# Optimization experiments

Hardware: AMD Instinct MI355X
Metric: run time of the kernel (lower is better)

The kernel has to match this reference:

```python
import jax, jax.numpy as jnp
import numpy as np

T, B, L, D, A = 64, 64, 100, 128, 18
H = 4 * D  # lstm_size = 4 * input_size


def lstm_cell(x, h, c, Wih, Whh, bih, bhh):
    # PyTorch LSTM gate order: i, f, g, o
    g = x @ Wih.T + bih + h @ Whh.T + bhh
    i, f, gg, o = jnp.split(g, 4, axis=-1)
    c = jax.nn.sigmoid(f) * c + jax.nn.sigmoid(i) * jnp.tanh(gg)
    h = jax.nn.sigmoid(o) * jnp.tanh(c)
    return h, c


def setup_inputs() -> dict:
    key = jax.random.key(0)
    ks = jax.random.split(key, 26)

    def gl(k, shape, fan_in):
        s = float(1.0 / np.sqrt(fan_in))
        return jax.random.uniform(k, shape, jnp.float32, -s, s)

    return dict(
        state=jax.random.normal(ks[0], (T, B, D), jnp.float32),
        demonstration=jax.random.normal(ks[1], (T, B, L, D), jnp.float32),
        demonstration_length=jax.random.randint(ks[2], (T, B), 1, L + 1),
        prev_action=jax.random.randint(ks[3], (T, B), 0, A),
        prev_reward=jax.random.normal(ks[4], (T, B), jnp.float32),
        h0=jnp.zeros((B, H), jnp.float32),
        c0=jnp.zeros((B, H), jnp.float32),
        enc_Wih=gl(ks[5], (4 * H, D), H), enc_Whh=gl(ks[6], (4 * H, H), H),
        enc_bih=gl(ks[7], (4 * H,), H), enc_bhh=gl(ks[8], (4 * H,), H),
        attn_W=gl(ks[9], (H, H), H), attn_b=gl(ks[10], (H,), H),
        comb_W=gl(ks[11], (H, D + H), D + H), comb_b=gl(ks[12], (H,), D + H),
        lstm_Wih=gl(ks[13], (4 * H, H), H), lstm_Whh=gl(ks[14], (4 * H, H), H),
        lstm_bih=gl(ks[15], (4 * H,), H), lstm_bhh=gl(ks[16], (4 * H,), H),
        mid_W=gl(ks[17], (H, H), H), mid_b=gl(ks[18], (H,), H),
        out_W=gl(ks[19], (A, H), H), out_b=gl(ks[20], (A,), H),
    )


def reference(state, demonstration, demonstration_length, prev_action, prev_reward,
              h0, c0, enc_Wih, enc_Whh, enc_bih, enc_bhh, attn_W, attn_b,
              comb_W, comb_b, lstm_Wih, lstm_Whh, lstm_bih, lstm_bhh,
              mid_W, mid_b, out_W, out_b):
    Lm = demonstration.shape[2]
    demo0 = demonstration[0]  # [B, L, D] (source uses demonstration[0] only)

    # --- demonstration encoder LSTM over L, zero initial state ---
    def enc_step(carry, x):
        h, c = carry
        h, c = lstm_cell(x, h, c, enc_Wih, enc_Whh, enc_bih, enc_bhh)
        return (h, c), h

    z = jnp.zeros((demo0.shape[0], H), demo0.dtype)
    _, enc = jax.lax.scan(enc_step, (z, z), jnp.swapaxes(demo0, 0, 1))
    enc = jnp.swapaxes(enc, 0, 1)  # [B, L, H]

    # invariant across t in the source loop; hoisted (same math)
    attn_proj = enc @ attn_W.T + attn_b  # [B, L, H]
    lengths = demonstration_length[0]  # [B]
    mask = jnp.arange(Lm)[None, :] < lengths[:, None]  # [B, L]
    scale = jnp.float32(1.0 / np.sqrt(Lm))

    # --- per-timestep fused attention + LSTM cell + heads ---
    def step(carry, obs_t):
        h, c = carry
        w = jnp.einsum('blh,bh->bl', attn_proj, h) * scale
        w = jnp.where(mask, w, -jnp.inf)
        w = jax.nn.softmax(w, axis=-1)
        applied = jnp.einsum('bl,blh->bh', w, enc)
        x = jax.nn.relu(jnp.concatenate([applied, obs_t], axis=-1) @ comb_W.T + comb_b)
        h, c = lstm_cell(x, h, c, lstm_Wih, lstm_Whh, lstm_bih, lstm_bhh)
        m = h @ mid_W.T + mid_b
        q_t = m @ out_W.T + out_b
        return (h, c), q_t

    (h, c), q = jax.lax.scan(step, (h0, c0), state)  # q: [T, B, A]
    return q, h, c
```

## Files before the change

### kernel.cpp

```cpp
#include <hip/hip_runtime.h>
#include <math.h>

#define Bsz 64
#define Tn 64
#define Ln 100
#define Dn 128
#define An 18
#define Hn 512
#define NGRP 16

__device__ __forceinline__ float sigf(float x){ return 1.0f/(1.0f+expf(-x)); }

__device__ __forceinline__ void scst(float* p, float v){
  __hip_atomic_store(p, v, __ATOMIC_RELAXED, __HIP_MEMORY_SCOPE_AGENT);
}
__device__ __forceinline__ void scsti(int* p, int v){
  __hip_atomic_store(p, v, __ATOMIC_RELAXED, __HIP_MEMORY_SCOPE_AGENT);
}
__device__ __forceinline__ int lcldi(const int* p){
  return __hip_atomic_load((int*)p, __ATOMIC_RELAXED, __HIP_MEMORY_SCOPE_AGENT);
}

__device__ __forceinline__ void gbar_arrive(int* grp_arr, int* grp_gen, int* root, int nb, int ph){
  const int gs = nb >> 4;
  const int g  = (int)blockIdx.x & 15;
  int a = __hip_atomic_fetch_add(grp_arr + g*64, 1, __ATOMIC_RELAXED, __HIP_MEMORY_SCOPE_AGENT) + 1;
  if (a == ph*gs){
    int r = __hip_atomic_fetch_add(root, 1, __ATOMIC_RELAXED, __HIP_MEMORY_SCOPE_AGENT) + 1;
    if (r == ph*NGRP){
      #pragma unroll
      for (int i = 0; i < NGRP; i++) scsti(grp_gen + i*64, ph);
    }
  }
}
__device__ __forceinline__ void gbar_wait(int* grp_gen, int ph){
  const int g = (int)blockIdx.x & 15;
  while (lcldi(grp_gen + g*64) < ph) __builtin_amdgcn_s_sleep(1);
}
__device__ __forceinline__ void gbarH(int* gA, int* gG, int* gR, int nb, int ph){
  __syncthreads();
  if (threadIdx.x == 0){
    asm volatile("s_waitcnt vmcnt(0) lgkmcnt(0)" ::: "memory");
    gbar_arrive(gA, gG, gR, nb, ph);
    gbar_wait(gG, ph);
  }
  __syncthreads();
}

__global__ __launch_bounds__(256) void demo_transpose_kernel(
    const float* __restrict__ demo, float* __restrict__ demoT)
{
  int idx = blockIdx.x*256 + threadIdx.x;
  if (idx < Ln*Bsz*Dn) {
    int d = idx & 127;
    int b = (idx >> 7) & 63;
    int l = idx >> 13;
    demoT[idx] = demo[((size_t)(b*Ln + l))*Dn + d];
  }
}

__global__ __launch_bounds__(256) void gemm_nt_kernel(
    const float* __restrict__ A, int lda,
    const float* __restrict__ B, int ldb,
    const float* __restrict__ bias,
    float* __restrict__ C, int ldc, int K)
{
  __shared__ float As[64][17];
  __shared__ float Bs[64][17];
  const int m0 = blockIdx.x * 64;
  const int n0 = blockIdx.y * 64;
  const int tx = threadIdx.x & 15;
  const int ty = threadIdx.x >> 4;
  float acc[4][4] = {};
  for (int k0 = 0; k0 < K; k0 += 16) {
    #pragma unroll
    for (int i = 0; i < 4; i++) {
      int e = threadIdx.x + i*256;
      int r = e >> 4, c = e & 15;
      As[r][c] = A[(size_t)(m0 + r)*lda + k0 + c];
      Bs[r][c] = B[(size_t)(n0 + r)*ldb + k0 + c];
    }
    __syncthreads();
    #pragma unroll
    for (int kk = 0; kk < 16; kk++) {
      float a0 = As[ty*4+0][kk], a1 = As[ty*4+1][kk], a2 = As[ty*4+2][kk], a3 = As[ty*4+3][kk];
      float b0 = Bs[tx*4+0][kk], b1 = Bs[tx*4+1][kk], b2 = Bs[tx*4+2][kk], b3 = Bs[tx*4+3][kk];
      acc[0][0] += a0*b0; acc[0][1] += a0*b1; acc[0][2] += a0*b2; acc[0][3] += a0*b3;
      acc[1][0] += a1*b0; acc[1][1] += a1*b1; acc[1][2] += a1*b2; acc[1][3] += a1*b3;
      acc[2][0] += a2*b0; acc[2][1] += a2*b1; acc[2][2] += a2*b2; acc[2][3] += a2*b3;
      acc[3][0] += a3*b0; acc[3][1] += a3*b1; acc[3][2] += a3*b2; acc[3][3] += a3*b3;
    }
    __syncthreads();
  }
  #pragma unroll
  for (int i = 0; i < 4; i++) {
    #pragma unroll
    for (int j = 0; j < 4; j++) {
      int nn = n0 + tx*4 + j;
      float v = acc[i][j] + (bias ? bias[nn] : 0.0f);
      C[(size_t)(m0 + ty*4 + i)*ldc + nn] = v;
    }
  }
}

__global__ __launch_bounds__(512) void head_fold_kernel(
    const float* __restrict__ mid_W, const float* __restrict__ mid_b,
    const float* __restrict__ out_W, const float* __restrict__ out_b,
    float* __restrict__ M2, float* __restrict__ bias2)
{
  const int a = blockIdx.x;
  const int k = threadIdx.x;
  const float* ow = out_W + (size_t)a*Hn;
  float s = 0.f;
  #pragma unroll 4
  for (int n = 0; n < Hn; n++) s += ow[n]*mid_W[(size_t)n*Hn + k];
  M2[(size_t)a*Hn + k] = s;
  if (k == 0){
    float b2 = out_b[a];
    for (int n = 0; n < Hn; n++) b2 += ow[n]*mid_b[n];
    bias2[a] = b2;
  }
}

__global__ __launch_bounds__(256) void qhead_kernel(
    const float* __restrict__ hhist, const float* __restrict__ M2,
    const float* __restrict__ bias2, float* __restrict__ q)
{
  const int t = blockIdx.x;
  for (int p = threadIdx.x; p < Bsz*An; p += 256){
    int b = p / An, a = p % An;
    const float4* hv = (const float4*)(hhist + ((size_t)t*Bsz + b)*Hn);
    const float4* mv = (const float4*)(M2 + (size_t)a*Hn);
    float s = bias2[a];
    #pragma unroll 8
    for (int k = 0; k < Hn/4; k++){
      float4 H = hv[k], M = mv[k];
      s += H.x*M.x + H.y*M.y + H.z*M.z + H.w*M.w;
    }
    q[((size_t)(t*Bsz + b))*An + a] = s;
  }
}

__global__ __launch_bounds__(512, 1) void enc_scan_kernel(
    const float* __restrict__ demoT,
    const float* __restrict__ Wih, const float* __restrict__ Whh,
    const float* __restrict__ bih, const float* __restrict__ bhh,
    const float* __restrict__ attn_W, const float* __restrict__ attn_b,
    const float* __restrict__ comb_W,
    float* __restrict__ hencR,
    float* __restrict__ attnp,
    float* __restrict__ CE,
    int* __restrict__ gA, int* __restrict__ gG, int* __restrict__ gR)
{
  const int bid  = blockIdx.x;
  const int tid  = threadIdx.x;
  const int lane = tid & 63;
  const int ks   = tid >> 6;
  const int n0   = bid*2;

  __shared__ float lds_whh[8][Hn];
  __shared__ float lds_wih[8][Dn];
  __shared__ float lds_atw[2][Hn];
  __shared__ float lds_cbw[2][Hn];
  __shared__ float red[8][12][Bsz];

  #pragma unroll
  for (int c = 0; c < 2; c++)
    #pragma unroll
    for (int g = 0; g < 4; g++){
      int r = c*4 + g;
      lds_whh[r][tid] = Whh[(size_t)(g*Hn + n0 + c)*Hn + tid];
      if (tid < Dn) lds_wih[r][tid] = Wih[(size_t)(g*Hn + n0 + c)*Dn + tid];
    }
  #pragma unroll
  for (int c = 0; c < 2; c++){
    lds_atw[c][tid] = attn_W[(size_t)(n0 + c)*Hn + tid];
    lds_cbw[c][tid] = comb_W[(size_t)(n0 + c)*(Hn + Dn) + tid];
  }
  float bsum[2][4];
  #pragma unroll
  for (int c = 0; c < 2; c++)
    #pragma unroll
    for (int g = 0; g < 4; g++){
      int r = g*Hn + n0 + c;
      bsum[c][g] = bih[r] + bhh[r];
    }
  const float ab[2] = { attn_b[n0], attn_b[n0+1] };
  float cr[2] = {0.f, 0.f};
  __syncthreads();

  for (int l = 0; l <= Ln; l++){
    float a[2][4] = {{0,0,0,0},{0,0,0,0}};
    float aa[2] = {0,0}, ac[2] = {0,0};
    if (l >= 1){
      const float4* hv = (const float4*)(hencR + ((size_t)(l-1)*Bsz + lane)*Hn) + ks*16;
      #pragma unroll 4
      for (int q = 0; q < 16; q++){
        float4 H = hv[q];
        #pragma unroll
        for (int c = 0; c < 2; c++){
          #pragma unroll
          for (int g = 0; g < 4; g++){
            float4 W = *(const float4*)&lds_whh[c*4+g][ks*64 + 4*q];
            a[c][g] += H.x*W.x + H.y*W.y + H.z*W.z + H.w*W.w;
          }
          float4 Aw = *(const float4*)&lds_atw[c][ks*64 + 4*q];
          aa[c] += H.x*Aw.x + H.y*Aw.y + H.z*Aw.z + H.w*Aw.w;
          float4 Cw = *(const float4*)&lds_cbw[c][ks*64 + 4*q];
          ac[c] += H.x*Cw.x + H.y*Cw.y + H.z*Cw.z + H.w*Cw.w;
        }
      }
    }
    if (l < Ln){
      const float4* dv = (const float4*)(demoT + ((size_t)l*Bsz + lane)*Dn) + ks*4;
      #pragma unroll
      for (int q = 0; q < 4; q++){
        float4 V = dv[q];
        #pragma unroll
        for (int c = 0; c < 2; c++)
          #pragma unroll
          for (int g = 0; g < 4; g++){
            float4 W = *(const float4*)&lds_wih[c*4+g][ks*16 + 4*q];
            a[c][g] += V.x*W.x + V.y*W.y + V.z*W.z + V.w*W.w;
          }
      }
    }
    #pragma unroll
    for (int c = 0; c < 2; c++){
      #pragma unroll
      for (int g = 0; g < 4; g++) red[ks][c*4+g][lane] = a[c][g];
      red[ks][8+c][lane]  = aa[c];
      red[ks][10+c][lane] = ac[c];
    }
    __syncthreads();
    if (tid < Bsz){
      int b = tid;
      if (l < Ln){
        #pragma unroll
        for (int c = 0; c < 2; c++){
          float g0 = bsum[c][0], g1 = bsum[c][1], g2 = bsum[c][2], g3 = bsum[c][3];
          #pragma unroll
          for (int k = 0; k < 8; k++){
            g0 += red[k][c*4+0][b]; g1 += red[k][c*4+1][b];
            g2 += red[k][c*4+2][b]; g3 += red[k][c*4+3][b];
          }
          float ii = sigf(g0), ff = sigf(g1), gg = tanhf(g2), oo = sigf(g3);
          float cn = ff*cr[c] + ii*gg;
          float hn = oo*tanhf(cn);
          cr[c] = cn;
          scst(hencR + ((size_t)l*Bsz + b)*Hn + n0 + c, hn);
        }
      }
      if (l >= 1){
        #pragma unroll
        for (int c = 0; c < 2; c++){
          float av = ab[c], cv = 0.f;
          #pragma unroll
          for (int k = 0; k < 8; k++){ av += red[k][8+c][b]; cv += red[k][10+c][b]; }
          scst(attnp + ((size_t)(b*Ln + (l-1)))*Hn + n0 + c, av);
          scst(CE    + ((size_t)(b*Ln + (l-1)))*Hn + n0 + c, cv);
        }
      }
    }
    if (l < Ln) gbarH(gA, gG, gR, (int)gridDim.x, l+1);
  }
}

__global__ __launch_bounds__(512, 1) void dec_scan_kernel(
    const float* __restrict__ h0, const float* __restrict__ c0,
    const float* __restrict__ attnp,
    const float* __restrict__ CE,
    const float* __restrict__ preobs,
    const int*   __restrict__ dlen,
    const float* __restrict__ lstm_Wih, const float* __restrict__ lstm_Whh,
    const float* __restrict__ lstm_bih, const float* __restrict__ lstm_bhh,
    const float* __restrict__ comb_b,
    float* __restrict__ xrow,
    float* __restrict__ hhist,
    float* __restrict__ outp,
    int* __restrict__ gA, int* __restrict__ gG, int* __restrict__ gR)
{
  const int bid  = blockIdx.x;
  const int tid  = threadIdx.x;
  const int lane = tid & 63;
  const int ks   = tid >> 6;
  const int n0   = bid*2;

  __shared__ float lds_wi[8][Hn];
  __shared__ float lds_wh[8][Hn];
  __shared__ float hs[Hn];
  __shared__ float wls[128];
  __shared__ float mx_s, sum_s;
  __shared__ float red[8][8][Bsz];

  #pragma unroll
  for (int c = 0; c < 2; c++)
    #pragma unroll
    for (int g = 0; g < 4; g++){
      int r = c*4 + g;
      lds_wi[r][tid] = lstm_Wih[(size_t)(g*Hn + n0 + c)*Hn + tid];
      lds_wh[r][tid] = lstm_Whh[(size_t)(g*Hn + n0 + c)*Hn + tid];
    }
  float bs[2][4];
  #pragma unroll
  for (int c = 0; c < 2; c++)
    #pragma unroll
    for (int g = 0; g < 4; g++){
      int r = g*Hn + n0 + c;
      bs[c][g] = lstm_bih[r] + lstm_bhh[r];
    }
  float cr[2] = {0.f, 0.f};
  int len = 0, lenr = 0;
  if (bid < Bsz){ len = dlen[bid]; lenr = (len + 7) & ~7; }
  int ph = 0;
  __syncthreads();

  for (int t = 0; t < Tn; t++){
    const float* hprev_all = (t == 0) ? h0 : (hhist + (size_t)(t-1)*Bsz*Hn);

    if (bid < Bsz){
      const int b = bid;
      hs[tid] = hprev_all[(size_t)b*Hn + tid];
      if (tid >= 100 && tid < 128) wls[tid] = -1e30f;
      __syncthreads();
      if (tid < 400){
        int l = tid >> 2, kh = tid & 3;
        const float4* ap = (const float4*)(attnp + ((size_t)(b*Ln + l))*Hn) + kh*32;
        const float4* hv = (const float4*)hs + kh*32;
        float s = 0.f;
        #pragma unroll 8
        for (int k = 0; k < 32; k++){
          float4 A = ap[k], H = hv[k];
          s += A.x*H.x + A.y*H.y + A.z*H.z + A.w*H.w;
        }
        s += __shfl_xor(s, 1);
        s += __shfl_xor(s, 2);
        if (kh == 0) wls[l] = (l < len) ? s*0.1f : -1e30f;
      }
      __syncthreads();
      if (tid < 64){
        float v = fmaxf(wls[tid], wls[tid+64]);
        for (int off = 1; off < 64; off <<= 1) v = fmaxf(v, __shfl_xor(v, off));
        if (tid == 0) mx_s = v;
      }
      __syncthreads();
      float mx = mx_s;
      if (tid < 64){
        float e0 = (wls[tid]    > -1e29f) ? expf(wls[tid]    - mx) : 0.f;
        float e1 = (wls[tid+64] > -1e29f) ? expf(wls[tid+64] - mx) : 0.f;
        wls[tid] = e0; wls[tid+64] = e1;
        float v = e0 + e1;
        for (int off = 1; off < 64; off <<= 1) v += __shfl_xor(v, off);
        if (tid == 0) sum_s = v;
      }
      __syncthreads();
      float inv = 1.0f / sum_s;
      {
        int n = tid;
        const float* cb = CE + (size_t)b*Ln*Hn + n;
        float acc = 0.f;
        #pragma unroll 8
        for (int l2 = 0; l2 < lenr; ++l2) acc += cb[(size_t)l2*Hn]*wls[l2];
        float v = acc*inv + preobs[((size_t)(t*Bsz + b))*Hn + n] + comb_b[n];
        scst(xrow + ((size_t)t*Bsz + b)*Hn + n, fmaxf(v, 0.f));
      }
    }
    float hpa[2][4] = {{0,0,0,0},{0,0,0,0}};
    {
      const float4* hv = (const float4*)(hprev_all + (size_t)lane*Hn) + ks*16;
      #pragma unroll 4
      for (int q = 0; q < 16; q++){
        float4 H = hv[q];
        #pragma unroll
        for (int c = 0; c < 2; c++)
          #pragma unroll
          for (int g = 0; g < 4; g++){
            float4 W = *(const float4*)&lds_wh[c*4+g][ks*64 + 4*q];
            hpa[c][g] += H.x*W.x + H.y*W.y + H.z*W.z + H.w*W.w;
          }
      }
    }
    gbarH(gA, gG, gR, (int)gridDim.x, ++ph);

    {
      const float4* xv = (const float4*)(xrow + ((size_t)t*Bsz + lane)*Hn) + ks*16;
      #pragma unroll 4
      for (int q = 0; q < 16; q++){
        float4 X = xv[q];
        #pragma unroll
        for (int c = 0; c < 2; c++)
          #pragma unroll
          for (int g = 0; g < 4; g++){
            float4 W = *(const float4*)&lds_wi[c*4+g][ks*64 + 4*q];
            hpa[c][g] += X.x*W.x + X.y*W.y + X.z*W.z + X.w*W.w;
          }
      }
      #pragma unroll
      for (int c = 0; c < 2; c++)
        #pragma unroll
        for (int g = 0; g < 4; g++) red[ks][c*4+g][lane] = hpa[c][g];
      __syncthreads();
      if (tid < Bsz){
        int b = tid;
        #pragma unroll
        for (int c = 0; c < 2; c++){
          int n = n0 + c;
          if (t == 0) cr[c] = c0[(size_t)b*Hn + n];
          float g0 = bs[c][0], g1 = bs[c][1], g2 = bs[c][2], g3 = bs[c][3];
          #pragma unroll
          for (int k = 0; k < 8; k++){
            g0 += red[k][c*4+0][b]; g1 += red[k][c*4+1][b];
            g2 += red[k][c*4+2][b]; g3 += red[k][c*4+3][b];
          }
          float ii = sigf(g0), ff = sigf(g1), gg = tanhf(g2), oo = sigf(g3);
          float cn = ff*cr[c] + ii*gg;
          float hn = oo*tanhf(cn);
          cr[c] = cn;
          scst(hhist + ((size_t)t*Bsz + b)*Hn + n, hn);
          if (t == Tn - 1){
            outp[Tn*Bsz*An + (size_t)b*Hn + n]           = hn;
            outp[Tn*Bsz*An + Bsz*Hn + (size_t)b*Hn + n]  = cn;
          }
        }
      }
    }
    if (t < Tn - 1) gbarH(gA, gG, gR, (int)gridDim.x, ++ph);
  }
}

extern "C" void kernel_launch(void* const* d_in, const int* in_sizes, int n_in,
                              void* d_out, int out_size, void* d_ws, size_t ws_size,
                              hipStream_t stream) {
  (void)in_sizes; (void)n_in; (void)out_size; (void)ws_size;
  const float* state    = (const float*)d_in[0];
  const float* demo     = (const float*)d_in[1];
  const int*   dlen     = (const int*)  d_in[2];
  const float* h0       = (const float*)d_in[5];
  const float* c0       = (const float*)d_in[6];
  const float* enc_Wih  = (const float*)d_in[7];
  const float* enc_Whh  = (const float*)d_in[8];
  const float* enc_bih  = (const float*)d_in[9];
  const float* enc_bhh  = (const float*)d_in[10];
  const float* attn_W   = (const float*)d_in[11];
  const float* attn_b   = (const float*)d_in[12];
  const float* comb_W   = (const float*)d_in[13];
  const float* comb_b   = (const float*)d_in[14];
  const float* lstm_Wih = (const float*)d_in[15];
  const float* lstm_Whh = (const float*)d_in[16];
  const float* lstm_bih = (const float*)d_in[17];
  const float* lstm_bhh = (const float*)d_in[18];
  const float* mid_W    = (const float*)d_in[19];
  const float* mid_b    = (const float*)d_in[20];
  const float* out_W    = (const float*)d_in[21];
  const float* out_b    = (const float*)d_in[22];
  float* ws   = (float*)d_ws;
  float* qout = (float*)d_out;

  float* attnp  = ws + 0;
  float* CE     = ws + 3276800;
  float* preobs = ws + 6555648;
  float* demoT  = ws + 8652800;
  float* hencR  = ws + 9472000;
  float* xrow   = ws + 12748800;
  float* hhist  = ws + 14845952;
  int*   barB   = (int*)(ws + 16943104);
  int* encA = barB;          int* encG = barB + 1024; int* encR = barB + 2048;
  int* decA = barB + 2112;   int* decG = barB + 3136; int* decR = barB + 4160;
  float* M2    = ws + 16947328;
  float* bias2 = ws + 16956544;

  hipMemsetAsync((void*)barB, 0, 4224*4, stream);

  demo_transpose_kernel<<<3200, 256, 0, stream>>>(demo, demoT);

  head_fold_kernel<<<An, 512, 0, stream>>>(mid_W, mid_b, out_W, out_b, M2, bias2);

  gemm_nt_kernel<<<dim3(Tn*Bsz/64, Hn/64), 256, 0, stream>>>(
      state, Dn, comb_W + Hn, Hn + Dn, nullptr, preobs, Hn, Dn);

  enc_scan_kernel<<<256, 512, 0, stream>>>(
      demoT, enc_Wih, enc_Whh, enc_bih, enc_bhh, attn_W, attn_b, comb_W,
      hencR, attnp, CE, encA, encG, encR);

  dec_scan_kernel<<<256, 512, 0, stream>>>(
      h0, c0, attnp, CE, preobs, dlen, lstm_Wih, lstm_Whh, lstm_bih, lstm_bhh,
      comb_b, xrow, hhist, qout, decA, decG, decR);

  qhead_kernel<<<Tn, 256, 0, stream>>>(hhist, M2, bias2, qout);
}
```

Before: 2.835 ms.

## Transpose combine-encoder buffer, batch-load hidden rows into registers, stagger attention reads

The encoder now stores the combine projection of encoder outputs transposed, as [B, H, Lpad] with L padded to 104. The decoder's attention-weighted sum can then read it as float4 along L instead of strided scalar loads. The recurrent matvecs in both scans load all 16 float4 hidden/input values into registers before the FMA loop, to expose more memory-level parallelism on the serial critical path. The attention score dot product staggers each thread's start offset to spread shared-memory bank access. Adjacent lanes now read addresses 104 floats apart rather than coalesced rows, and the padding entries past L=100 are never written, so the code relies on zero softmax weights multiplying whatever sits there.

```diff
diff --git a/kernel.cpp b/kernel.cpp
--- a/kernel.cpp
+++ b/kernel.cpp
@@ -4,6 +4,7 @@
 #define Bsz 64
 #define Tn 64
 #define Ln 100
+#define Lpad 104
 #define Dn 128
 #define An 18
 #define Hn 512
@@ -149,7 +150,7 @@
     const float* __restrict__ comb_W,
     float* __restrict__ hencR,
     float* __restrict__ attnp,
-    float* __restrict__ CE,
+    float* __restrict__ ceT,
     int* __restrict__ gA, int* __restrict__ gG, int* __restrict__ gR)
 {
   const int bid  = blockIdx.x;
@@ -194,20 +195,22 @@
     float aa[2] = {0,0}, ac[2] = {0,0};
     if (l >= 1){
       const float4* hv = (const float4*)(hencR + ((size_t)(l-1)*Bsz + lane)*Hn) + ks*16;
-      #pragma unroll 4
+      float4 H[16];
+      #pragma unroll
+      for (int q = 0; q < 16; q++) H[q] = hv[q];
+      #pragma unroll
       for (int q = 0; q < 16; q++){
-        float4 H = hv[q];
         #pragma unroll
         for (int c = 0; c < 2; c++){
           #pragma unroll
           for (int g = 0; g < 4; g++){
             float4 W = *(const float4*)&lds_whh[c*4+g][ks*64 + 4*q];
-            a[c][g] += H.x*W.x + H.y*W.y + H.z*W.z + H.w*W.w;
+            a[c][g] += H[q].x*W.x + H[q].y*W.y + H[q].z*W.z + H[q].w*W.w;
           }
           float4 Aw = *(const float4*)&lds_atw[c][ks*64 + 4*q];
-          aa[c] += H.x*Aw.x + H.y*Aw.y + H.z*Aw.z + H.w*Aw.w;
+          aa[c] += H[q].x*Aw.x + H[q].y*Aw.y + H[q].z*Aw.z + H[q].w*Aw.w;
           float4 Cw = *(const float4*)&lds_cbw[c][ks*64 + 4*q];
-          ac[c] += H.x*Cw.x + H.y*Cw.y + H.z*Cw.z + H.w*Cw.w;
+          ac[c] += H[q].x*Cw.x + H[q].y*Cw.y + H[q].z*Cw.z + H[q].w*Cw.w;
         }
       }
     }
@@ -258,7 +261,7 @@
           #pragma unroll
           for (int k = 0; k < 8; k++){ av += red[k][8+c][b]; cv += red[k][10+c][b]; }
           scst(attnp + ((size_t)(b*Ln + (l-1)))*Hn + n0 + c, av);
-          scst(CE    + ((size_t)(b*Ln + (l-1)))*Hn + n0 + c, cv);
+          scst(ceT   + ((size_t)(b*Hn + n0 + c))*Lpad + (l-1), cv);
         }
       }
     }
@@ -269,7 +272,7 @@
 __global__ __launch_bounds__(512, 1) void dec_scan_kernel(
     const float* __restrict__ h0, const float* __restrict__ c0,
     const float* __restrict__ attnp,
-    const float* __restrict__ CE,
+    const float* __restrict__ ceT,
     const float* __restrict__ preobs,
     const int*   __restrict__ dlen,
     const float* __restrict__ lstm_Wih, const float* __restrict__ lstm_Whh,
@@ -288,8 +291,8 @@
 
   __shared__ float lds_wi[8][Hn];
   __shared__ float lds_wh[8][Hn];
-  __shared__ float hs[Hn];
-  __shared__ float wls[128];
+  __shared__ __align__(16) float hs[Hn];
+  __shared__ __align__(16) float wls[128];
   __shared__ float mx_s, sum_s;
   __shared__ float red[8][8][Bsz];
 
@@ -325,12 +328,13 @@
       __syncthreads();
       if (tid < 400){
         int l = tid >> 2, kh = tid & 3;
-        const float4* ap = (const float4*)(attnp + ((size_t)(b*Ln + l))*Hn) + kh*32;
-        const float4* hv = (const float4*)hs + kh*32;
+        const float4* ap = (const float4*)(attnp + ((size_t)(b*Ln + l))*Hn);
+        const float4* hv = (const float4*)hs;
         float s = 0.f;
         #pragma unroll 8
         for (int k = 0; k < 32; k++){
-          float4 A = ap[k], H = hv[k];
+          int j = kh*32 + ((k + 2*kh) & 31);
+          float4 A = ap[j], H = hv[j];
           s += A.x*H.x + A.y*H.y + A.z*H.z + A.w*H.w;
         }
         s += __shfl_xor(s, 1);
@@ -357,10 +361,15 @@
       float inv = 1.0f / sum_s;
       {
         int n = tid;
-        const float* cb = CE + (size_t)b*Ln*Hn + n;
+        const float4* cb4 = (const float4*)(ceT + ((size_t)b*Hn + n)*Lpad);
         float acc = 0.f;
-        #pragma unroll 8
-        for (int l2 = 0; l2 < lenr; ++l2) acc += cb[(size_t)l2*Hn]*wls[l2];
+        int l4 = lenr >> 2;
+        #pragma unroll 4
+        for (int j = 0; j < l4; ++j){
+          float4 C4 = cb4[j];
+          float4 W4 = *(const float4*)&wls[4*j];
+          acc += C4.x*W4.x + C4.y*W4.y + C4.z*W4.z + C4.w*W4.w;
+        }
         float v = acc*inv + preobs[((size_t)(t*Bsz + b))*Hn + n] + comb_b[n];
         scst(xrow + ((size_t)t*Bsz + b)*Hn + n, fmaxf(v, 0.f));
       }
@@ -368,15 +377,17 @@
     float hpa[2][4] = {{0,0,0,0},{0,0,0,0}};
     {
       const float4* hv = (const float4*)(hprev_all + (size_t)lane*Hn) + ks*16;
-      #pragma unroll 4
+      float4 H[16];
+      #pragma unroll
+      for (int q = 0; q < 16; q++) H[q] = hv[q];
+      #pragma unroll
       for (int q = 0; q < 16; q++){
-        float4 H = hv[q];
         #pragma unroll
         for (int c = 0; c < 2; c++)
           #pragma unroll
           for (int g = 0; g < 4; g++){
             float4 W = *(const float4*)&lds_wh[c*4+g][ks*64 + 4*q];
-            hpa[c][g] += H.x*W.x + H.y*W.y + H.z*W.z + H.w*W.w;
+            hpa[c][g] += H[q].x*W.x + H[q].y*W.y + H[q].z*W.z + H[q].w*W.w;
           }
       }
     }
@@ -384,15 +395,17 @@
 
     {
       const float4* xv = (const float4*)(xrow + ((size_t)t*Bsz + lane)*Hn) + ks*16;
-      #pragma unroll 4
+      float4 X[16];
+      #pragma unroll
+      for (int q = 0; q < 16; q++) X[q] = xv[q];
+      #pragma unroll
       for (int q = 0; q < 16; q++){
-        float4 X = xv[q];
         #pragma unroll
         for (int c = 0; c < 2; c++)
           #pragma unroll
           for (int g = 0; g < 4; g++){
             float4 W = *(const float4*)&lds_wi[c*4+g][ks*64 + 4*q];
-            hpa[c][g] += X.x*W.x + X.y*W.y + X.z*W.z + X.w*W.w;
+            hpa[c][g] += X[q].x*W.x + X[q].y*W.y + X[q].z*W.z + X[q].w*W.w;
           }
       }
       #pragma unroll
@@ -457,17 +470,17 @@
   float* qout = (float*)d_out;
 
   float* attnp  = ws + 0;
-  float* CE     = ws + 3276800;
-  float* preobs = ws + 6555648;
-  float* demoT  = ws + 8652800;
-  float* hencR  = ws + 9472000;
-  float* xrow   = ws + 12748800;
-  float* hhist  = ws + 14845952;
-  int*   barB   = (int*)(ws + 16943104);
+  float* ceT    = ws + 3276800;
+  float* preobs = ws + 6684672;
+  float* demoT  = ws + 8781824;
+  float* hencR  = ws + 9601024;
+  float* xrow   = ws + 12877824;
+  float* hhist  = ws + 14974976;
+  int*   barB   = (int*)(ws + 17072128);
   int* encA = barB;          int* encG = barB + 1024; int* encR = barB + 2048;
   int* decA = barB + 2112;   int* decG = barB + 3136; int* decR = barB + 4160;
-  float* M2    = ws + 16947328;
-  float* bias2 = ws + 16956544;
+  float* M2    = ws + 17076352;
+  float* bias2 = ws + 17085568;
 
   hipMemsetAsync((void*)barB, 0, 4224*4, stream);
 
@@ -480,10 +493,10 @@
 
   enc_scan_kernel<<<256, 512, 0, stream>>>(
       demoT, enc_Wih, enc_Whh, enc_bih, enc_bhh, attn_W, attn_b, comb_W,
-      hencR, attnp, CE, encA, encG, encR);
+      hencR, attnp, ceT, encA, encG, encR);
 
   dec_scan_kernel<<<256, 512, 0, stream>>>(
-      h0, c0, attnp, CE, preobs, dlen, lstm_Wih, lstm_Whh, lstm_bih, lstm_bhh,
+      h0, c0, attnp, ceT, preobs, dlen, lstm_Wih, lstm_Whh, lstm_bih, lstm_bhh,
       comb_b, xrow, hhist, qout, decA, decG, decR);
 
   qhead_kernel<<<Tn, 256, 0, stream>>>(hhist, M2, bias2, qout);
```

Result: slower. 8.517 ms (+200.5%).

## Fold transpose, preobs GEMM, head fold and q-head into the persistent scan kernels

Applied to the files above, without the earlier changes.

Removes four small kernel launches (demo transpose, state×comb_W GEMM, head folding, q-head) by moving their work into the prologue and epilogue of the two persistent cooperative scan kernels. Each prologue ends in an extra grid barrier so that dependent data is visible. The q-head now runs after a final grid barrier and uses a per-wave shuffle reduction. This saves launch gaps and intermediate kernel boundaries, but adds grid-barrier phases and runs the GEMM with a naive per-thread dot product instead of a tiled LDS GEMM.

```diff
diff --git a/kernel.cpp b/kernel.cpp
--- a/kernel.cpp
+++ b/kernel.cpp
@@ -47,106 +47,13 @@
   __syncthreads();
 }
 
-__global__ __launch_bounds__(256) void demo_transpose_kernel(
-    const float* __restrict__ demo, float* __restrict__ demoT)
-{
-  int idx = blockIdx.x*256 + threadIdx.x;
-  if (idx < Ln*Bsz*Dn) {
-    int d = idx & 127;
-    int b = (idx >> 7) & 63;
-    int l = idx >> 13;
-    demoT[idx] = demo[((size_t)(b*Ln + l))*Dn + d];
-  }
-}
-
-__global__ __launch_bounds__(256) void gemm_nt_kernel(
-    const float* __restrict__ A, int lda,
-    const float* __restrict__ B, int ldb,
-    const float* __restrict__ bias,
-    float* __restrict__ C, int ldc, int K)
-{
-  __shared__ float As[64][17];
-  __shared__ float Bs[64][17];
-  const int m0 = blockIdx.x * 64;
-  const int n0 = blockIdx.y * 64;
-  const int tx = threadIdx.x & 15;
-  const int ty = threadIdx.x >> 4;
-  float acc[4][4] = {};
-  for (int k0 = 0; k0 < K; k0 += 16) {
-    #pragma unroll
-    for (int i = 0; i < 4; i++) {
-      int e = threadIdx.x + i*256;
-      int r = e >> 4, c = e & 15;
-      As[r][c] = A[(size_t)(m0 + r)*lda + k0 + c];
-      Bs[r][c] = B[(size_t)(n0 + r)*ldb + k0 + c];
-    }
-    __syncthreads();
-    #pragma unroll
-    for (int kk = 0; kk < 16; kk++) {
-      float a0 = As[ty*4+0][kk], a1 = As[ty*4+1][kk], a2 = As[ty*4+2][kk], a3 = As[ty*4+3][kk];
-      float b0 = Bs[tx*4+0][kk], b1 = Bs[tx*4+1][kk], b2 = Bs[tx*4+2][kk], b3 = Bs[tx*4+3][kk];
-      acc[0][0] += a0*b0; acc[0][1] += a0*b1; acc[0][2] += a0*b2; acc[0][3] += a0*b3;
-      acc[1][0] += a1*b0; acc[1][1] += a1*b1; acc[1][2] += a1*b2; acc[1][3] += a1*b3;
-      acc[2][0] += a2*b0; acc[2][1] += a2*b1; acc[2][2] += a2*b2; acc[2][3] += a2*b3;
-      acc[3][0] += a3*b0; acc[3][1] += a3*b1; acc[3][2] += a3*b2; acc[3][3] += a3*b3;
-    }
-    __syncthreads();
-  }
-  #pragma unroll
-  for (int i = 0; i < 4; i++) {
-    #pragma unroll
-    for (int j = 0; j < 4; j++) {
-      int nn = n0 + tx*4 + j;
-      float v = acc[i][j] + (bias ? bias[nn] : 0.0f);
-      C[(size_t)(m0 + ty*4 + i)*ldc + nn] = v;
-    }
-  }
-}
-
-__global__ __launch_bounds__(512) void head_fold_kernel(
-    const float* __restrict__ mid_W, const float* __restrict__ mid_b,
-    const float* __restrict__ out_W, const float* __restrict__ out_b,
-    float* __restrict__ M2, float* __restrict__ bias2)
-{
-  const int a = blockIdx.x;
-  const int k = threadIdx.x;
-  const float* ow = out_W + (size_t)a*Hn;
-  float s = 0.f;
-  #pragma unroll 4
-  for (int n = 0; n < Hn; n++) s += ow[n]*mid_W[(size_t)n*Hn + k];
-  M2[(size_t)a*Hn + k] = s;
-  if (k == 0){
-    float b2 = out_b[a];
-    for (int n = 0; n < Hn; n++) b2 += ow[n]*mid_b[n];
-    bias2[a] = b2;
-  }
-}
-
-__global__ __launch_bounds__(256) void qhead_kernel(
-    const float* __restrict__ hhist, const float* __restrict__ M2,
-    const float* __restrict__ bias2, float* __restrict__ q)
-{
-  const int t = blockIdx.x;
-  for (int p = threadIdx.x; p < Bsz*An; p += 256){
-    int b = p / An, a = p % An;
-    const float4* hv = (const float4*)(hhist + ((size_t)t*Bsz + b)*Hn);
-    const float4* mv = (const float4*)(M2 + (size_t)a*Hn);
-    float s = bias2[a];
-    #pragma unroll 8
-    for (int k = 0; k < Hn/4; k++){
-      float4 H = hv[k], M = mv[k];
-      s += H.x*M.x + H.y*M.y + H.z*M.z + H.w*M.w;
-    }
-    q[((size_t)(t*Bsz + b))*An + a] = s;
-  }
-}
-
 __global__ __launch_bounds__(512, 1) void enc_scan_kernel(
-    const float* __restrict__ demoT,
+    const float* __restrict__ demo,
     const float* __restrict__ Wih, const float* __restrict__ Whh,
     const float* __restrict__ bih, const float* __restrict__ bhh,
     const float* __restrict__ attn_W, const float* __restrict__ attn_b,
     const float* __restrict__ comb_W,
+    float* __restrict__ demoT,
     float* __restrict__ hencR,
     float* __restrict__ attnp,
     float* __restrict__ CE,
@@ -187,7 +94,19 @@
     }
   const float ab[2] = { attn_b[n0], attn_b[n0+1] };
   float cr[2] = {0.f, 0.f};
-  __syncthreads();
+  int pe = 0;
+
+  {
+    const int base = bid*3200;
+    for (int i = tid; i < 3200; i += 512){
+      int idx = base + i;
+      int d  = idx & 127;
+      int b2 = (idx >> 7) & 63;
+      int l2 = idx >> 13;
+      scst(demoT + idx, demo[((size_t)(b2*Ln + l2))*Dn + d]);
+    }
+    gbarH(gA, gG, gR, (int)gridDim.x, ++pe);
+  }
 
   for (int l = 0; l <= Ln; l++){
     float a[2][4] = {{0,0,0,0},{0,0,0,0}};
@@ -262,19 +181,24 @@
         }
       }
     }
-    if (l < Ln) gbarH(gA, gG, gR, (int)gridDim.x, l+1);
+    if (l < Ln) gbarH(gA, gG, gR, (int)gridDim.x, ++pe);
   }
 }
 
 __global__ __launch_bounds__(512, 1) void dec_scan_kernel(
     const float* __restrict__ h0, const float* __restrict__ c0,
+    const float* __restrict__ state,
     const float* __restrict__ attnp,
     const float* __restrict__ CE,
-    const float* __restrict__ preobs,
     const int*   __restrict__ dlen,
     const float* __restrict__ lstm_Wih, const float* __restrict__ lstm_Whh,
     const float* __restrict__ lstm_bih, const float* __restrict__ lstm_bhh,
-    const float* __restrict__ comb_b,
+    const float* __restrict__ comb_W,  const float* __restrict__ comb_b,
+    const float* __restrict__ mid_W,   const float* __restrict__ mid_b,
+    const float* __restrict__ out_W,   const float* __restrict__ out_b,
+    float* __restrict__ preobs,
+    float* __restrict__ M2,
+    float* __restrict__ bias2,
     float* __restrict__ xrow,
     float* __restrict__ hhist,
     float* __restrict__ outp,
@@ -288,8 +212,8 @@
 
   __shared__ float lds_wi[8][Hn];
   __shared__ float lds_wh[8][Hn];
-  __shared__ float hs[Hn];
-  __shared__ float wls[128];
+  __shared__ __align__(16) float hs[Hn];
+  __shared__ __align__(16) float wls[128];
   __shared__ float mx_s, sum_s;
   __shared__ float red[8][8][Bsz];
 
@@ -313,7 +237,43 @@
   int len = 0, lenr = 0;
   if (bid < Bsz){ len = dlen[bid]; lenr = (len + 7) & ~7; }
   int ph = 0;
-  __syncthreads();
+
+  {
+    if (tid < Dn){
+      hs[tid]      = comb_W[(size_t)n0*(Hn+Dn)     + Hn + tid];
+      hs[Dn + tid] = comb_W[(size_t)(n0+1)*(Hn+Dn) + Hn + tid];
+    }
+    __syncthreads();
+    #pragma unroll
+    for (int p = 0; p < 8; p++){
+      int r = p*512 + tid;
+      const float4* sv = (const float4*)(state + (size_t)r*Dn);
+      const float4* w0 = (const float4*)hs;
+      const float4* w1 = (const float4*)(hs + Dn);
+      float a0 = 0.f, a1 = 0.f;
+      #pragma unroll 8
+      for (int q = 0; q < 32; q++){
+        float4 S = sv[q], W0 = w0[q], W1 = w1[q];
+        a0 += S.x*W0.x + S.y*W0.y + S.z*W0.z + S.w*W0.w;
+        a1 += S.x*W1.x + S.y*W1.y + S.z*W1.z + S.w*W1.w;
+      }
+      scst(preobs + (size_t)r*Hn + n0,     a0);
+      scst(preobs + (size_t)r*Hn + n0 + 1, a1);
+    }
+    if (bid < An){
+      const float* ow = out_W + (size_t)bid*Hn;
+      float s = 0.f;
+      #pragma unroll 4
+      for (int n = 0; n < Hn; n++) s += ow[n]*mid_W[(size_t)n*Hn + tid];
+      scst(M2 + (size_t)bid*Hn + tid, s);
+      if (tid == 0){
+        float b2 = out_b[bid];
+        for (int n = 0; n < Hn; n++) b2 += ow[n]*mid_b[n];
+        scst(bias2 + bid, b2);
+      }
+    }
+    gbarH(gA, gG, gR, (int)gridDim.x, ++ph);
+  }
 
   for (int t = 0; t < Tn; t++){
     const float* hprev_all = (t == 0) ? h0 : (hhist + (size_t)(t-1)*Bsz*Hn);
@@ -424,7 +384,24 @@
         }
       }
     }
-    if (t < Tn - 1) gbarH(gA, gG, gR, (int)gridDim.x, ++ph);
+    gbarH(gA, gG, gR, (int)gridDim.x, ++ph);
+  }
+
+  {
+    const int tq = bid & 63;
+    const int qd = bid >> 6;
+    for (int j = 0; j < 36; j++){
+      int oi = qd*288 + ks*36 + j;
+      int b = oi / An, a = oi % An;
+      const float4* hv = (const float4*)(hhist + ((size_t)tq*Bsz + b)*Hn) + lane*2;
+      const float4* mv = (const float4*)(M2 + (size_t)a*Hn) + lane*2;
+      float4 H0 = hv[0], H1 = hv[1], M0 = mv[0], M1 = mv[1];
+      float s = H0.x*M0.x + H0.y*M0.y + H0.z*M0.z + H0.w*M0.w
+              + H1.x*M1.x + H1.y*M1.y + H1.z*M1.z + H1.w*M1.w;
+      #pragma unroll
+      for (int off = 1; off < 64; off <<= 1) s += __shfl_xor(s, off);
+      if (lane == 0) outp[((size_t)tq*Bsz + b)*An + a] = s + bias2[a];
+    }
   }
 }
 
@@ -471,20 +448,12 @@
 
   hipMemsetAsync((void*)barB, 0, 4224*4, stream);
 
-  demo_transpose_kernel<<<3200, 256, 0, stream>>>(demo, demoT);
-
-  head_fold_kernel<<<An, 512, 0, stream>>>(mid_W, mid_b, out_W, out_b, M2, bias2);
-
-  gemm_nt_kernel<<<dim3(Tn*Bsz/64, Hn/64), 256, 0, stream>>>(
-      state, Dn, comb_W + Hn, Hn + Dn, nullptr, preobs, Hn, Dn);
-
   enc_scan_kernel<<<256, 512, 0, stream>>>(
-      demoT, enc_Wih, enc_Whh, enc_bih, enc_bhh, attn_W, attn_b, comb_W,
-      hencR, attnp, CE, encA, encG, encR);
+      demo, enc_Wih, enc_Whh, enc_bih, enc_bhh, attn_W, attn_b, comb_W,
+      demoT, hencR, attnp, CE, encA, encG, encR);
 
   dec_scan_kernel<<<256, 512, 0, stream>>>(
-      h0, c0, attnp, CE, preobs, dlen, lstm_Wih, lstm_Whh, lstm_bih, lstm_bhh,
-      comb_b, xrow, hhist, qout, decA, decG, decR);
-
-  qhead_kernel<<<Tn, 256, 0, stream>>>(hhist, M2, bias2, qout);
-}
+      h0, c0, state, attnp, CE, dlen, lstm_Wih, lstm_Whh, lstm_bih, lstm_bhh,
+      comb_W, comb_b, mid_W, mid_b, out_W, out_b,
+      preobs, M2, bias2, xrow, hhist, qout, decA, decG, decR);
+}
```

Measured after the change: 2.823 ms. About the same (-0.4%).
